# Kernel tuning notes

Measured on AMD Instinct MI355X. Metric: run time of the kernel, lower is better.

Reference implementation:

```python
import jax, jax.numpy as jnp
import numpy as np
import math

D_MODEL = 1024
NUM_HEADS = 16
D_K = D_MODEL // NUM_HEADS
B, S = 4, 1024


def setup_inputs() -> dict:
    key = jax.random.key(0)
    ks = jax.random.split(key, 12)
    std = 1.0 / math.sqrt(D_MODEL)
    inp = {
        "query": jax.random.normal(ks[0], (B, S, D_MODEL), jnp.float32),
        "key": jax.random.normal(ks[1], (B, S, D_MODEL), jnp.float32),
        "value": jax.random.normal(ks[2], (B, S, D_MODEL), jnp.float32),
        "time_diffs": jax.random.uniform(ks[3], (B, S, S), jnp.float32),
        "mask": jnp.ones((B, 1, S, S), jnp.int32),
        # learned params (torch Linear: y = x @ W.T + b; here W stored as [in, out])
        "Wq": jax.random.normal(ks[4], (D_MODEL, D_MODEL), jnp.float32) * std,
        "bq": jnp.zeros((D_MODEL,), jnp.float32),
        "Wk": jax.random.normal(ks[5], (D_MODEL, D_MODEL), jnp.float32) * std,
        "bk": jnp.zeros((D_MODEL,), jnp.float32),
        "Wv": jax.random.normal(ks[6], (D_MODEL, D_MODEL), jnp.float32) * std,
        "bv": jnp.zeros((D_MODEL,), jnp.float32),
        "Wt": jax.random.normal(ks[7], (D_K,), jnp.float32),  # Linear(1, d_k) weight, flattened
        "bt": jax.random.normal(ks[8], (D_K,), jnp.float32) * 0.02,
        "Wo": jax.random.normal(ks[9], (D_MODEL, D_MODEL), jnp.float32) * std,
        "bo": jnp.zeros((D_MODEL,), jnp.float32),
    }
    return inp


def reference(query, key, value, time_diffs, mask, Wq, bq, Wk, bk, Wv, bv, Wt, bt, Wo, bo):
    b = query.shape[0]
    # project and split heads: [B, H, S, Dk]
    def split_heads(x):
        return x.reshape(b, -1, NUM_HEADS, D_K).transpose(0, 2, 1, 3)

    q = split_heads(query @ Wq + bq)
    k = split_heads(key @ Wk + bk)
    v = split_heads(value @ Wv + bv)

    scores = jnp.einsum("bhqd,bhkd->bhqk", q, k) / math.sqrt(D_K)

    # time_proj(t)[...,j] = t*Wt[j] + bt[j]; sum over j == t*sum(Wt) + sum(bt)
    time_decay = time_diffs * jnp.sum(Wt) + jnp.sum(bt)  # [B, S, S]
    scores = scores - time_decay[:, None, :, :]

    scores = jnp.where(mask == 0, jnp.float32(-1e9), scores)
    attn = jax.nn.softmax(scores, axis=-1)  # dropout is identity in eval

    out = jnp.einsum("bhqk,bhkd->bhqd", attn, v)
    out = out.transpose(0, 2, 1, 3).reshape(b, -1, D_MODEL)
    return out @ Wo + bo
```

## Files before the change

### kernel.cpp

```cpp
#include <hip/hip_runtime.h>
#include <stdint.h>
#include <stddef.h>


typedef __attribute__((ext_vector_type(4))) float f32x4;
typedef __attribute__((ext_vector_type(16))) float f32x16;
typedef __attribute__((ext_vector_type(8))) short bf16x8;
typedef __attribute__((ext_vector_type(4))) short short4v;
typedef __attribute__((ext_vector_type(4))) float float4v;
typedef __attribute__((ext_vector_type(4))) unsigned int u32x4;

constexpr int NHEAD = 16;
constexpr int DKV = 64;
constexpr int DMODEL = 1024;
constexpr int SEQ = 1024;

__device__ __forceinline__ short f2bf(float f) {
  uint32_t u = __builtin_bit_cast(uint32_t, f);
  uint32_t r = (u + 0x7fffu + ((u >> 16) & 1u)) >> 16;
  return (short)r;
}
__device__ __forceinline__ float bf2f(short s) {
  uint32_t u = ((uint32_t)(unsigned short)s) << 16;
  return __builtin_bit_cast(float, u);
}

__device__ __forceinline__ void gload_lds16(const void* g, void* l) {
  __builtin_amdgcn_global_load_lds(
      (const __attribute__((address_space(1))) void*)g,
      (__attribute__((address_space(3))) void*)l, 16, 0, 0);
}

__device__ __forceinline__ void plane_swap(unsigned int& a, unsigned int& b) {
#if __has_builtin(__builtin_amdgcn_permlane32_swap)
  auto r = __builtin_amdgcn_permlane32_swap(a, b, false, false);
  a = r[0];
  b = r[1];
#else
  unsigned int sa = (unsigned int)__shfl_xor((int)a, 32);
  unsigned int sb = (unsigned int)__shfl_xor((int)b, 32);
  bool hi = (threadIdx.x & 32) != 0;
  unsigned int na = hi ? sb : a;
  unsigned int nb = hi ? b : sa;
  a = na;
  b = nb;
#endif
}

__global__ __launch_bounds__(256) void convert3_kernel(
    const float* __restrict__ q, const float* __restrict__ k,
    const float* __restrict__ v, short* __restrict__ oq,
    short* __restrict__ ok, short* __restrict__ ov) {
  const float* src = blockIdx.y == 0 ? q : (blockIdx.y == 1 ? k : v);
  short* dst = blockIdx.y == 0 ? oq : (blockIdx.y == 1 ? ok : ov);
  int i = blockIdx.x * 256 + threadIdx.x;
  const float4v* s = (const float4v*)src;
  float4v a = s[2 * i];
  float4v b = s[2 * i + 1];
  bf16x8 o;
  o[0] = f2bf(a[0]); o[1] = f2bf(a[1]); o[2] = f2bf(a[2]); o[3] = f2bf(a[3]);
  o[4] = f2bf(b[0]); o[5] = f2bf(b[1]); o[6] = f2bf(b[2]); o[7] = f2bf(b[3]);
  ((bf16x8*)dst)[i] = o;
}

__global__ void transposeW_kernel(const float* __restrict__ W0,
                                  const float* __restrict__ W1,
                                  const float* __restrict__ W2,
                                  const float* __restrict__ W3,
                                  short* __restrict__ T0, short* __restrict__ T1,
                                  short* __restrict__ T2,
                                  short* __restrict__ T3) {
  const float* W = blockIdx.z == 0 ? W0
                   : (blockIdx.z == 1 ? W1 : (blockIdx.z == 2 ? W2 : W3));
  short* Wt = blockIdx.z == 0 ? T0
              : (blockIdx.z == 1 ? T1 : (blockIdx.z == 2 ? T2 : T3));
  __shared__ float t[32][33];
  int tx = threadIdx.x, ty = threadIdx.y;
  int bx = blockIdx.x * 32, by = blockIdx.y * 32;
  t[ty][tx] = W[(size_t)(by + ty) * DMODEL + bx + tx];
  __syncthreads();
  Wt[(size_t)(bx + ty) * DMODEL + by + tx] = f2bf(t[tx][ty]);
}

__device__ __forceinline__ void gemm_swz(int f, int& tm, int& tn) {
  int y = (f & 7) * 8 + ((f >> 3) & 7);
  int x = f >> 6;
  tm = y * 64;
  tn = x * 128;
}

template <int MODE>
__device__ __forceinline__ void gemm_bt_body(const short* __restrict__ A,
                                             const short* __restrict__ Bt,
                                             const float* __restrict__ bias,
                                             void* __restrict__ Cptr, int K,
                                             float oscale, int tm, int tn,
                                             short* __restrict__ As,
                                             short* __restrict__ Bs) {
  const int tid = threadIdx.x;
  const int wave = tid >> 6;
  const int lane = tid & 63;
  const int wm = (wave >> 1) * 32;
  const int wn = (wave & 1) * 64;
  const int frow = lane & 15;
  const int lg = lane >> 4;

  f32x4 acc[2][4];
#pragma unroll
  for (int i = 0; i < 2; ++i)
#pragma unroll
    for (int j = 0; j < 4; ++j) acc[i][j] = (f32x4){0.f, 0.f, 0.f, 0.f};

  const int sa0 = tid, sa1 = tid + 256;
  const int ar0 = sa0 >> 3, ac0 = (sa0 & 7) ^ (ar0 & 7);
  const int ar1 = sa1 >> 3, ac1 = (sa1 & 7) ^ (ar1 & 7);
  const short* asrc0 = A + (size_t)(tm + ar0) * K + ac0 * 8;
  const short* asrc1 = A + (size_t)(tm + ar1) * K + ac1 * 8;
  short* adst0 = &As[(wave * 64) * 8];
  short* adst1 = &As[(256 + wave * 64) * 8];

  int brr[4], bcc[4];
  const short* bsrc[4];
  short* bdst[4];
#pragma unroll
  for (int q = 0; q < 4; ++q) {
    int s = q * 256 + tid;
    brr[q] = s >> 3;
    bcc[q] = (s & 7) ^ (brr[q] & 7);
    bsrc[q] = Bt + (size_t)(tn + brr[q]) * K + bcc[q] * 8;
    bdst[q] = &Bs[(q * 256 + wave * 64) * 8];
  }

  for (int k0 = 0; k0 < K; k0 += 64) {
    __syncthreads();
    gload_lds16(asrc0 + k0, adst0);
    gload_lds16(asrc1 + k0, adst1);
#pragma unroll
    for (int q = 0; q < 4; ++q) gload_lds16(bsrc[q] + k0, bdst[q]);
    asm volatile("s_waitcnt vmcnt(0)" ::: "memory");
    __syncthreads();

#pragma unroll
    for (int kk = 0; kk < 2; ++kk) {
      bf16x8 af[2], bfr[4];
      int lc = kk * 4 + lg;
#pragma unroll
      for (int mf = 0; mf < 2; ++mf) {
        int row = wm + mf * 16 + frow;
        af[mf] = *(const bf16x8*)((const char*)As + row * 128 +
                                  ((lc ^ (row & 7)) * 16));
      }
#pragma unroll
      for (int nf = 0; nf < 4; ++nf) {
        int row = wn + nf * 16 + frow;
        bfr[nf] = *(const bf16x8*)((const char*)Bs + row * 128 +
                                   ((lc ^ (row & 7)) * 16));
      }
#pragma unroll
      for (int mf = 0; mf < 2; ++mf)
#pragma unroll
        for (int nf = 0; nf < 4; ++nf)
          acc[mf][nf] = __builtin_amdgcn_mfma_f32_16x16x32_bf16(
              af[mf], bfr[nf], acc[mf][nf], 0, 0, 0);
    }
  }

  const int crow = lg * 4;
  const int ccol = frow;
#pragma unroll
  for (int mf = 0; mf < 2; ++mf) {
#pragma unroll
    for (int nf = 0; nf < 4; ++nf) {
      int n = tn + wn + nf * 16 + ccol;
      float bv = bias[n];
      if (MODE == 2) {
        int m0r = tm + wm + mf * 16 + crow;
        int b = m0r >> 10, s0 = m0r & 1023;
        int hh = n >> 6, d = n & 63;
        short4v pk;
#pragma unroll
        for (int r = 0; r < 4; ++r) pk[r] = f2bf(acc[mf][nf][r] + bv);
        *(short4v*)&((short*)Cptr)[((size_t)((b * NHEAD + hh) * DKV + d)) * SEQ +
                                   s0] = pk;
      } else {
#pragma unroll
        for (int r = 0; r < 4; ++r) {
          int m = tm + wm + mf * 16 + crow + r;
          float v = acc[mf][nf][r] + bv;
          if (MODE == 0) {
            int b = m >> 10, s = m & 1023;
            int hh = n >> 6, d = n & 63;
            ((short*)Cptr)[(((size_t)(b * NHEAD + hh)) * SEQ + s) * DKV + d] =
                f2bf(v * oscale);
          } else {
            ((float*)Cptr)[(size_t)m * DMODEL + n] = v;
          }
        }
      }
    }
  }
}

__global__ __launch_bounds__(256) void qkv_gemm_kernel(
    const short* __restrict__ Xq, const short* __restrict__ Xk,
    const short* __restrict__ Xv, const short* __restrict__ Wqt,
    const short* __restrict__ Wkt, const short* __restrict__ Wvt,
    const float* __restrict__ bq, const float* __restrict__ bk,
    const float* __restrict__ bv, short* __restrict__ Qh,
    short* __restrict__ Kh, short* __restrict__ VhT) {
  __shared__ short As[64 * 64];
  __shared__ short Bs[128 * 64];
  int tm, tn;
  gemm_swz(blockIdx.x, tm, tn);
  int z = blockIdx.y;
  if (z == 2) {
    gemm_bt_body<2>(Xv, Wvt, bv, VhT, DMODEL, 1.0f, tm, tn, As, Bs);
  } else if (z == 1) {
    gemm_bt_body<0>(Xk, Wkt, bk, Kh, DMODEL, 1.0f, tm, tn, As, Bs);
  } else {
    gemm_bt_body<0>(Xq, Wqt, bq, Qh, DMODEL, 0.125f * 1.44269504088896f, tm,
                    tn, As, Bs);
  }
}

__global__ __launch_bounds__(256) void out_gemm_kernel(
    const short* __restrict__ Ao, const short* __restrict__ Wot,
    const float* __restrict__ bo, float* __restrict__ out) {
  __shared__ short As[64 * 64];
  __shared__ short Bs[128 * 64];
  int tm, tn;
  gemm_swz(blockIdx.x, tm, tn);
  gemm_bt_body<1>(Ao, Wot, bo, out, DMODEL, 1.0f, tm, tn, As, Bs);
}

__global__ __launch_bounds__(512) void attn_kernel(
    const short* __restrict__ Qh, const short* __restrict__ Kh,
    const short* __restrict__ VhT, const float* __restrict__ Tdif,
    const float* __restrict__ WtP, short* __restrict__ Oh) {
  __shared__ short Ks[2][64 * 64];
  __shared__ short Vts[2][64 * 64];

  const int tid = threadIdx.x;
  const int wave = tid >> 6;
  const int lane = tid & 63;
  const int lq = lane & 31;
  const int hi = lane >> 5;
  const int bid = blockIdx.x;
  const int swz = (bid & 7) * 32 + (bid >> 3);
  const int bh = swz >> 2;
  const int b = bh >> 4;
  const int h = bh & 15;
  const int q0 = (swz & 3) * 256;
  const int qrow = q0 + wave * 32 + lq;

  float sWt = WtP[lane];
#pragma unroll
  for (int sh = 1; sh < 64; sh <<= 1) sWt += __shfl_xor(sWt, sh);
  sWt *= 1.44269504088896f;

  bf16x8 qf[4];
  {
    const short* qb = Qh + ((size_t)bh * SEQ + qrow) * DKV + hi * 8;
#pragma unroll
    for (int ks = 0; ks < 4; ++ks) qf[ks] = *(const bf16x8*)(qb + ks * 16);
  }

  float m_run = -1e30f, l_run = 0.f;
  f32x16 o2[2];
#pragma unroll
  for (int db = 0; db < 2; ++db)
#pragma unroll
    for (int r = 0; r < 16; ++r) o2[db][r] = 0.f;

  const int r0 = tid >> 3;
  const int c0 = (tid & 7) ^ (r0 & 7);
  const short* kbase = Kh + (size_t)bh * SEQ * DKV;
  const short* vtbase = VhT + (size_t)bh * DKV * SEQ;
  const float* tdf = Tdif + ((size_t)(b * SEQ) + qrow) * SEQ;

  for (int kt2 = 0; kt2 < 8; ++kt2) {
    const int kb0 = kt2 * 128;
    __syncthreads();
#pragma unroll
    for (int half = 0; half < 2; ++half) {
      const int kb = kb0 + half * 64;
      gload_lds16(kbase + (size_t)(kb + r0) * DKV + c0 * 8,
                  &Ks[half][wave * 512]);
      gload_lds16(vtbase + (size_t)r0 * SEQ + kb + c0 * 8,
                  &Vts[half][wave * 512]);
    }
    asm volatile("s_waitcnt vmcnt(0)" ::: "memory");
    __syncthreads();

    float4v tdb[4][4];
#pragma unroll
    for (int kq = 0; kq < 4; ++kq)
#pragma unroll
      for (int c = 0; c < 4; ++c)
        tdb[kq][c] = *(const float4v*)(tdf + kb0 + kq * 32 + c * 8 + hi * 4);

    f32x16 sc2[4];
#pragma unroll
    for (int kq = 0; kq < 4; ++kq)
#pragma unroll
      for (int r = 0; r < 16; ++r) sc2[kq][r] = 0.f;
    __builtin_amdgcn_s_setprio(1);
#pragma unroll
    for (int kq = 0; kq < 4; ++kq) {
      int half = kq >> 1, kb2 = kq & 1;
#pragma unroll
      for (int s = 0; s < 4; ++s) {
        int key = kb2 * 32 + lq;
        int kbyte = (key * 128 + s * 32 + hi * 16) ^ ((key & 7) << 4);
        bf16x8 kfrag = *(const bf16x8*)((const char*)Ks[half] + kbyte);
        sc2[kq] = __builtin_amdgcn_mfma_f32_32x32x16_bf16(kfrag, qf[s],
                                                          sc2[kq], 0, 0, 0);
      }
    }
    __builtin_amdgcn_s_setprio(0);

#pragma unroll
    for (int kq = 0; kq < 4; ++kq)
#pragma unroll
      for (int r = 0; r < 16; ++r)
        sc2[kq][r] -= tdb[kq][r >> 2][r & 3] * sWt;

    float t16[16];
#pragma unroll
    for (int r = 0; r < 16; ++r)
      t16[r] = fmaxf(fmaxf(sc2[0][r], sc2[1][r]), fmaxf(sc2[2][r], sc2[3][r]));
    float t8[8], t4[4];
#pragma unroll
    for (int r = 0; r < 8; ++r) t8[r] = fmaxf(t16[r], t16[r + 8]);
#pragma unroll
    for (int r = 0; r < 4; ++r) t4[r] = fmaxf(t8[r], t8[r + 4]);
    float mx = fmaxf(fmaxf(t4[0], t4[1]), fmaxf(t4[2], t4[3]));
    mx = fmaxf(mx, __shfl_xor(mx, 32));

    if (!__all(mx <= m_run + 8.f)) {
      float mnew = fmaxf(m_run, mx);
      float scl = exp2f(m_run - mnew);
      l_run *= scl;
#pragma unroll
      for (int db = 0; db < 2; ++db)
#pragma unroll
        for (int r = 0; r < 16; ++r) o2[db][r] *= scl;
      m_run = mnew;
    }

    float ssum = 0.f;
    unsigned int u[4][4][2];
#pragma unroll
    for (int kq = 0; kq < 4; ++kq)
#pragma unroll
      for (int c = 0; c < 4; ++c) {
        float p0 = exp2f(sc2[kq][c * 4 + 0] - m_run);
        float p1 = exp2f(sc2[kq][c * 4 + 1] - m_run);
        float p2 = exp2f(sc2[kq][c * 4 + 2] - m_run);
        float p3 = exp2f(sc2[kq][c * 4 + 3] - m_run);
        unsigned int lo, hi2;
        asm("v_cvt_pk_bf16_f32 %0, %1, %2" : "=v"(lo) : "v"(p0), "v"(p1));
        asm("v_cvt_pk_bf16_f32 %0, %1, %2" : "=v"(hi2) : "v"(p2), "v"(p3));
        u[kq][c][0] = lo;
        u[kq][c][1] = hi2;
        ssum += __builtin_bit_cast(float, lo << 16) +
                __builtin_bit_cast(float, lo & 0xffff0000u) +
                __builtin_bit_cast(float, hi2 << 16) +
                __builtin_bit_cast(float, hi2 & 0xffff0000u);
      }
    ssum += __shfl_xor(ssum, 32);
    l_run += ssum;

    __builtin_amdgcn_s_setprio(1);
#pragma unroll
    for (int half = 0; half < 2; ++half) {
#pragma unroll
      for (int ks = 0; ks < 4; ++ks) {
        int kq = half * 2 + (ks >> 1), c0i = (ks & 1) * 2;
        unsigned int a0 = u[kq][c0i][0], b0 = u[kq][c0i + 1][0];
        unsigned int a1 = u[kq][c0i][1], b1 = u[kq][c0i + 1][1];
        plane_swap(a0, b0);
        plane_swap(a1, b1);
        u32x4 pw = {a0, a1, b0, b1};
        bf16x8 pf = __builtin_bit_cast(bf16x8, pw);
#pragma unroll
        for (int db = 0; db < 2; ++db) {
          int d = db * 32 + lq;
          int vbyte = (d * 128 + ks * 32 + hi * 16) ^ ((d & 7) << 4);
          bf16x8 vfrag = *(const bf16x8*)((const char*)Vts[half] + vbyte);
          o2[db] = __builtin_amdgcn_mfma_f32_32x32x16_bf16(vfrag, pf, o2[db],
                                                           0, 0, 0);
        }
      }
    }
    __builtin_amdgcn_s_setprio(0);
  }

  float invl = 1.f / l_run;
  short* orow = Oh + ((size_t)b * SEQ + qrow) * DMODEL + h * DKV;
#pragma unroll
  for (int db = 0; db < 2; ++db)
#pragma unroll
    for (int c = 0; c < 4; ++c) {
      short4v s4;
#pragma unroll
      for (int i = 0; i < 4; ++i) s4[i] = f2bf(o2[db][c * 4 + i] * invl);
      int d = db * 32 + c * 8 + hi * 4;
      *(short4v*)(orow + d) = s4;
    }
}

extern "C" void kernel_launch(void* const* d_in, const int* in_sizes, int n_in,
                              void* d_out, int out_size, void* d_ws,
                              size_t ws_size, hipStream_t stream) {
  const float* query = (const float*)d_in[0];
  const float* key_ = (const float*)d_in[1];
  const float* value = (const float*)d_in[2];
  const float* tdif = (const float*)d_in[3];
  const float* Wq = (const float*)d_in[5];
  const float* bq = (const float*)d_in[6];
  const float* Wk = (const float*)d_in[7];
  const float* bk = (const float*)d_in[8];
  const float* Wv = (const float*)d_in[9];
  const float* bv = (const float*)d_in[10];
  const float* Wt = (const float*)d_in[11];
  const float* Wo = (const float*)d_in[13];
  const float* bo = (const float*)d_in[14];

  char* w = (char*)d_ws;
  const size_t SZX = (size_t)4096 * 1024 * 2;
  const size_t SZW = (size_t)1024 * 1024 * 2;
  short* Xq = (short*)(w);
  short* Xk = (short*)(w + SZX);
  short* Xv = (short*)(w + 2 * SZX);
  short* Wqt = (short*)(w + 3 * SZX);
  short* Wkt = (short*)(w + 3 * SZX + SZW);
  short* Wvt = (short*)(w + 3 * SZX + 2 * SZW);
  short* Wot = (short*)(w + 3 * SZX + 3 * SZW);
  short* Qh = (short*)(w + 3 * SZX + 4 * SZW);
  short* Kh = (short*)(w + 4 * SZX + 4 * SZW);
  short* VhT = (short*)(w + 5 * SZX + 4 * SZW);
  short* Ao = (short*)(w + 6 * SZX + 4 * SZW);

  convert3_kernel<<<dim3(2048, 3), 256, 0, stream>>>(query, key_, value, Xq, Xk,
                                                     Xv);
  transposeW_kernel<<<dim3(32, 32, 4), dim3(32, 32), 0, stream>>>(
      Wq, Wk, Wv, Wo, Wqt, Wkt, Wvt, Wot);
  qkv_gemm_kernel<<<dim3(512, 3), 256, 0, stream>>>(
      Xq, Xk, Xv, Wqt, Wkt, Wvt, bq, bk, bv, Qh, Kh, VhT);
  attn_kernel<<<dim3(256), 512, 0, stream>>>(Qh, Kh, VhT, tdif, Wt, Ao);
  out_gemm_kernel<<<dim3(512), 256, 0, stream>>>(Ao, Wot, bo, (float*)d_out);
}
```

Baseline: 125.8 us.

## Split attention KV range across two wave groups with LDS merge of partials

The attention kernel now handles 128 query rows per block instead of 256. Its eight waves form two groups, each covering half of the key/value sequence (split-K flash attention). The grid doubles to 512 blocks to fill more CUs, and the partial max, sum and output are merged through shared memory at the end. This doubles LDS buffers to 32KB per tile set, and Q fragments are loaded by two waves each. It also adds a final LDS merge and an extra barrier.

```diff
diff --git a/kernel.cpp b/kernel.cpp
--- a/kernel.cpp
+++ b/kernel.cpp
@@ -4,6 +4,7 @@
 
 
 typedef __attribute__((ext_vector_type(4))) float f32x4;
+typedef __attribute__((ext_vector_type(2))) float f32x2;
 typedef __attribute__((ext_vector_type(16))) float f32x16;
 typedef __attribute__((ext_vector_type(8))) short bf16x8;
 typedef __attribute__((ext_vector_type(4))) short short4v;
@@ -233,25 +234,28 @@
   gemm_bt_body<1>(Ao, Wot, bo, out, DMODEL, 1.0f, tm, tn, As, Bs);
 }
 
-__global__ __launch_bounds__(512) void attn_kernel(
+__global__ __launch_bounds__(512, 4) void attn_kernel(
     const short* __restrict__ Qh, const short* __restrict__ Kh,
     const short* __restrict__ VhT, const float* __restrict__ Tdif,
     const float* __restrict__ WtP, short* __restrict__ Oh) {
-  __shared__ short Ks[2][64 * 64];
-  __shared__ short Vts[2][64 * 64];
+  __shared__ short Ks[4][64 * 64];
+  __shared__ short Vts[4][64 * 64];
 
   const int tid = threadIdx.x;
   const int wave = tid >> 6;
   const int lane = tid & 63;
   const int lq = lane & 31;
   const int hi = lane >> 5;
+  const int sub = wave & 3;
+  const int half = wave >> 2;
   const int bid = blockIdx.x;
-  const int swz = (bid & 7) * 32 + (bid >> 3);
-  const int bh = swz >> 2;
+  const int swz = (bid & 7) * 64 + (bid >> 3);
+  const int bh = swz >> 3;
   const int b = bh >> 4;
   const int h = bh & 15;
-  const int q0 = (swz & 3) * 256;
-  const int qrow = q0 + wave * 32 + lq;
+  const int q0 = (swz & 7) * 128;
+  const int qrow = q0 + sub * 32 + lq;
+  const int kvofs = half * 512;
 
   float sWt = WtP[lane];
 #pragma unroll
@@ -278,107 +282,106 @@
   const short* vtbase = VhT + (size_t)bh * DKV * SEQ;
   const float* tdf = Tdif + ((size_t)(b * SEQ) + qrow) * SEQ;
 
-  for (int kt2 = 0; kt2 < 8; ++kt2) {
-    const int kb0 = kt2 * 128;
+  for (int it = 0; it < 4; ++it) {
     __syncthreads();
 #pragma unroll
-    for (int half = 0; half < 2; ++half) {
-      const int kb = kb0 + half * 64;
+    for (int t4 = 0; t4 < 4; ++t4) {
+      const int kb = (t4 >> 1) * 512 + it * 128 + (t4 & 1) * 64;
       gload_lds16(kbase + (size_t)(kb + r0) * DKV + c0 * 8,
-                  &Ks[half][wave * 512]);
+                  &Ks[t4][wave * 512]);
       gload_lds16(vtbase + (size_t)r0 * SEQ + kb + c0 * 8,
-                  &Vts[half][wave * 512]);
+                  &Vts[t4][wave * 512]);
     }
     asm volatile("s_waitcnt vmcnt(0)" ::: "memory");
     __syncthreads();
 
-    float4v tdb[4][4];
-#pragma unroll
-    for (int kq = 0; kq < 4; ++kq)
-#pragma unroll
-      for (int c = 0; c < 4; ++c)
-        tdb[kq][c] = *(const float4v*)(tdf + kb0 + kq * 32 + c * 8 + hi * 4);
-
-    f32x16 sc2[4];
-#pragma unroll
-    for (int kq = 0; kq < 4; ++kq)
-#pragma unroll
-      for (int r = 0; r < 16; ++r) sc2[kq][r] = 0.f;
-    __builtin_amdgcn_s_setprio(1);
-#pragma unroll
-    for (int kq = 0; kq < 4; ++kq) {
-      int half = kq >> 1, kb2 = kq & 1;
-#pragma unroll
-      for (int s = 0; s < 4; ++s) {
-        int key = kb2 * 32 + lq;
-        int kbyte = (key * 128 + s * 32 + hi * 16) ^ ((key & 7) << 4);
-        bf16x8 kfrag = *(const bf16x8*)((const char*)Ks[half] + kbyte);
-        sc2[kq] = __builtin_amdgcn_mfma_f32_32x32x16_bf16(kfrag, qf[s],
-                                                          sc2[kq], 0, 0, 0);
-      }
-    }
-    __builtin_amdgcn_s_setprio(0);
-
-#pragma unroll
-    for (int kq = 0; kq < 4; ++kq)
-#pragma unroll
-      for (int r = 0; r < 16; ++r)
-        sc2[kq][r] -= tdb[kq][r >> 2][r & 3] * sWt;
-
-    float t16[16];
-#pragma unroll
-    for (int r = 0; r < 16; ++r)
-      t16[r] = fmaxf(fmaxf(sc2[0][r], sc2[1][r]), fmaxf(sc2[2][r], sc2[3][r]));
-    float t8[8], t4[4];
-#pragma unroll
-    for (int r = 0; r < 8; ++r) t8[r] = fmaxf(t16[r], t16[r + 8]);
-#pragma unroll
-    for (int r = 0; r < 4; ++r) t4[r] = fmaxf(t8[r], t8[r + 4]);
-    float mx = fmaxf(fmaxf(t4[0], t4[1]), fmaxf(t4[2], t4[3]));
-    mx = fmaxf(mx, __shfl_xor(mx, 32));
-
-    if (!__all(mx <= m_run + 8.f)) {
-      float mnew = fmaxf(m_run, mx);
-      float scl = exp2f(m_run - mnew);
-      l_run *= scl;
-#pragma unroll
-      for (int db = 0; db < 2; ++db)
-#pragma unroll
-        for (int r = 0; r < 16; ++r) o2[db][r] *= scl;
-      m_run = mnew;
-    }
-
-    float ssum = 0.f;
-    unsigned int u[4][4][2];
-#pragma unroll
-    for (int kq = 0; kq < 4; ++kq)
-#pragma unroll
-      for (int c = 0; c < 4; ++c) {
-        float p0 = exp2f(sc2[kq][c * 4 + 0] - m_run);
-        float p1 = exp2f(sc2[kq][c * 4 + 1] - m_run);
-        float p2 = exp2f(sc2[kq][c * 4 + 2] - m_run);
-        float p3 = exp2f(sc2[kq][c * 4 + 3] - m_run);
-        unsigned int lo, hi2;
-        asm("v_cvt_pk_bf16_f32 %0, %1, %2" : "=v"(lo) : "v"(p0), "v"(p1));
-        asm("v_cvt_pk_bf16_f32 %0, %1, %2" : "=v"(hi2) : "v"(p2), "v"(p3));
-        u[kq][c][0] = lo;
-        u[kq][c][1] = hi2;
-        ssum += __builtin_bit_cast(float, lo << 16) +
-                __builtin_bit_cast(float, lo & 0xffff0000u) +
-                __builtin_bit_cast(float, hi2 << 16) +
-                __builtin_bit_cast(float, hi2 & 0xffff0000u);
-      }
-    ssum += __shfl_xor(ssum, 32);
-    l_run += ssum;
-
-    __builtin_amdgcn_s_setprio(1);
-#pragma unroll
-    for (int half = 0; half < 2; ++half) {
+#pragma unroll
+    for (int t = 0; t < 2; ++t) {
+      const int buf = half * 2 + t;
+      const int kb = kvofs + it * 128 + t * 64;
+      float4v tdb[2][4];
+#pragma unroll
+      for (int kb2 = 0; kb2 < 2; ++kb2)
+#pragma unroll
+        for (int c = 0; c < 4; ++c)
+          tdb[kb2][c] =
+              *(const float4v*)(tdf + kb + kb2 * 32 + c * 8 + hi * 4);
+
+      f32x16 sc2[2];
+#pragma unroll
+      for (int kb2 = 0; kb2 < 2; ++kb2)
+#pragma unroll
+        for (int r = 0; r < 16; ++r) sc2[kb2][r] = 0.f;
+      __builtin_amdgcn_s_setprio(1);
+#pragma unroll
+      for (int kb2 = 0; kb2 < 2; ++kb2)
+#pragma unroll
+        for (int s = 0; s < 4; ++s) {
+          int key = kb2 * 32 + lq;
+          int kbyte = (key * 128 + s * 32 + hi * 16) ^ ((key & 7) << 4);
+          bf16x8 kfrag = *(const bf16x8*)((const char*)Ks[buf] + kbyte);
+          sc2[kb2] = __builtin_amdgcn_mfma_f32_32x32x16_bf16(kfrag, qf[s],
+                                                             sc2[kb2], 0, 0, 0);
+        }
+      __builtin_amdgcn_s_setprio(0);
+
+#pragma unroll
+      for (int kb2 = 0; kb2 < 2; ++kb2)
+#pragma unroll
+        for (int r = 0; r < 16; ++r)
+          sc2[kb2][r] -= tdb[kb2][r >> 2][r & 3] * sWt;
+
+      float t16[16];
+#pragma unroll
+      for (int r = 0; r < 16; ++r) t16[r] = fmaxf(sc2[0][r], sc2[1][r]);
+      float t8[8], t4x[4];
+#pragma unroll
+      for (int r = 0; r < 8; ++r) t8[r] = fmaxf(t16[r], t16[r + 8]);
+#pragma unroll
+      for (int r = 0; r < 4; ++r) t4x[r] = fmaxf(t8[r], t8[r + 4]);
+      float mx = fmaxf(fmaxf(t4x[0], t4x[1]), fmaxf(t4x[2], t4x[3]));
+      mx = fmaxf(mx, __shfl_xor(mx, 32));
+
+      if (!__all(mx <= m_run + 8.f)) {
+        float mnew = fmaxf(m_run, mx);
+        float scl = exp2f(m_run - mnew);
+        l_run *= scl;
+#pragma unroll
+        for (int db = 0; db < 2; ++db)
+#pragma unroll
+          for (int r = 0; r < 16; ++r) o2[db][r] *= scl;
+        m_run = mnew;
+      }
+
+      float ssum = 0.f;
+      unsigned int u[2][4][2];
+#pragma unroll
+      for (int kb2 = 0; kb2 < 2; ++kb2)
+#pragma unroll
+        for (int c = 0; c < 4; ++c) {
+          float p0 = exp2f(sc2[kb2][c * 4 + 0] - m_run);
+          float p1 = exp2f(sc2[kb2][c * 4 + 1] - m_run);
+          float p2 = exp2f(sc2[kb2][c * 4 + 2] - m_run);
+          float p3 = exp2f(sc2[kb2][c * 4 + 3] - m_run);
+          unsigned int lo, hi2;
+          asm("v_cvt_pk_bf16_f32 %0, %1, %2" : "=v"(lo) : "v"(p0), "v"(p1));
+          asm("v_cvt_pk_bf16_f32 %0, %1, %2" : "=v"(hi2) : "v"(p2), "v"(p3));
+          u[kb2][c][0] = lo;
+          u[kb2][c][1] = hi2;
+          ssum += __builtin_bit_cast(float, lo << 16) +
+                  __builtin_bit_cast(float, lo & 0xffff0000u) +
+                  __builtin_bit_cast(float, hi2 << 16) +
+                  __builtin_bit_cast(float, hi2 & 0xffff0000u);
+        }
+      ssum += __shfl_xor(ssum, 32);
+      l_run += ssum;
+
+      __builtin_amdgcn_s_setprio(1);
 #pragma unroll
       for (int ks = 0; ks < 4; ++ks) {
-        int kq = half * 2 + (ks >> 1), c0i = (ks & 1) * 2;
-        unsigned int a0 = u[kq][c0i][0], b0 = u[kq][c0i + 1][0];
-        unsigned int a1 = u[kq][c0i][1], b1 = u[kq][c0i + 1][1];
+        int kb2 = ks >> 1, c0i = (ks & 1) * 2;
+        unsigned int a0 = u[kb2][c0i][0], b0 = u[kb2][c0i + 1][0];
+        unsigned int a1 = u[kb2][c0i][1], b1 = u[kb2][c0i + 1][1];
         plane_swap(a0, b0);
         plane_swap(a1, b1);
         u32x4 pw = {a0, a1, b0, b1};
@@ -387,27 +390,50 @@
         for (int db = 0; db < 2; ++db) {
           int d = db * 32 + lq;
           int vbyte = (d * 128 + ks * 32 + hi * 16) ^ ((d & 7) << 4);
-          bf16x8 vfrag = *(const bf16x8*)((const char*)Vts[half] + vbyte);
+          bf16x8 vfrag = *(const bf16x8*)((const char*)Vts[buf] + vbyte);
           o2[db] = __builtin_amdgcn_mfma_f32_32x32x16_bf16(vfrag, pf, o2[db],
                                                            0, 0, 0);
         }
       }
-    }
-    __builtin_amdgcn_s_setprio(0);
-  }
-
-  float invl = 1.f / l_run;
-  short* orow = Oh + ((size_t)b * SEQ + qrow) * DMODEL + h * DKV;
-#pragma unroll
-  for (int db = 0; db < 2; ++db)
-#pragma unroll
-    for (int c = 0; c < 4; ++c) {
+      __builtin_amdgcn_s_setprio(0);
+    }
+  }
+
+  __syncthreads();
+  float4v* mbufO = (float4v*)&Ks[0][0];
+  f32x2* mbufML = (f32x2*)&Vts[0][0];
+  if (half == 1) {
+    int reg = (wave - 4) * 64 + lane;
+#pragma unroll
+    for (int c = 0; c < 8; ++c) {
+      float4v v = {o2[c >> 2][(c & 3) * 4 + 0], o2[c >> 2][(c & 3) * 4 + 1],
+                   o2[c >> 2][(c & 3) * 4 + 2], o2[c >> 2][(c & 3) * 4 + 3]};
+      mbufO[c * 256 + reg] = v;
+    }
+    mbufML[reg] = (f32x2){m_run, l_run};
+  }
+  __syncthreads();
+  if (half == 0) {
+    int reg = wave * 64 + lane;
+    f32x2 ml2 = mbufML[reg];
+    float m = fmaxf(m_run, ml2[0]);
+    float w1 = exp2f(m_run - m), w2 = exp2f(ml2[0] - m);
+    float invl = 1.f / (l_run * w1 + ml2[1] * w2);
+    short* orow = Oh + ((size_t)b * SEQ + qrow) * DMODEL + h * DKV;
+#pragma unroll
+    for (int c = 0; c < 8; ++c) {
+      float4v v2 = mbufO[c * 256 + reg];
       short4v s4;
 #pragma unroll
-      for (int i = 0; i < 4; ++i) s4[i] = f2bf(o2[db][c * 4 + i] * invl);
-      int d = db * 32 + c * 8 + hi * 4;
+      for (int i = 0; i < 4; ++i) {
+        float o1 = o2[c >> 2][(c & 3) * 4 + i];
+        s4[i] = f2bf((o1 * w1 + v2[i] * w2) * invl);
+      }
+      int db = c >> 2, cc = c & 3;
+      int d = db * 32 + cc * 8 + hi * 4;
       *(short4v*)(orow + d) = s4;
     }
+  }
 }
 
 extern "C" void kernel_launch(void* const* d_in, const int* in_sizes, int n_in,
@@ -448,6 +474,6 @@
       Wq, Wk, Wv, Wo, Wqt, Wkt, Wvt, Wot);
   qkv_gemm_kernel<<<dim3(512, 3), 256, 0, stream>>>(
       Xq, Xk, Xv, Wqt, Wkt, Wvt, bq, bk, bv, Qh, Kh, VhT);
-  attn_kernel<<<dim3(256), 512, 0, stream>>>(Qh, Kh, VhT, tdif, Wt, Ao);
+  attn_kernel<<<dim3(512), 512, 0, stream>>>(Qh, Kh, VhT, tdif, Wt, Ao);
   out_gemm_kernel<<<dim3(512), 256, 0, stream>>>(Ao, Wot, bo, (float*)d_out);
 }
```

After: 174.2 us. 1.38x slower.
